# Kernel tuning notes

Measured on AMD Instinct MI355X. Metric: run time of the kernel, lower is better.

## Reference

```python
import jax, jax.numpy as jnp
import numpy as np

NUM_RADIAL = 16
HIDDEN = 128
OUT_DIM = 128
N_LAYERS = 3
N_NODES = 20000
N_EDGES = 640000


def _orthogonal(key, rows, cols):
    # mimic nn.init.orthogonal_ for a [rows, cols] weight
    n = max(rows, cols)
    a = jax.random.normal(key, (n, min(rows, cols)), dtype=jnp.float32)
    q, r = jnp.linalg.qr(a)
    q = q * jnp.sign(jnp.diagonal(r))  # make deterministic-ish sign
    w = q[:rows, :cols] if rows >= cols else q[:cols, :rows].T
    return w.astype(jnp.float32)


def setup_inputs() -> dict:
    key = jax.random.key(0)
    ks = jax.random.split(key, 8)
    distance_representation = jax.random.normal(ks[0], (N_EDGES, NUM_RADIAL), dtype=jnp.float32)
    message = jax.random.normal(ks[1], (N_EDGES, HIDDEN), dtype=jnp.float32)
    edge_index = jax.random.randint(ks[2], (2, N_EDGES), 0, N_NODES, dtype=jnp.int32)
    # parameters (torch Linear stores weight as [out, in])
    Wd = _orthogonal(ks[3], HIDDEN, NUM_RADIAL)          # linear_distance.weight
    layer_keys = jax.random.split(ks[4], N_LAYERS)
    Ws = jnp.stack([_orthogonal(k, HIDDEN, HIDDEN) for k in layer_keys])  # [L, H, H]
    bs = jnp.zeros((N_LAYERS, HIDDEN), dtype=jnp.float32)
    Wout = _orthogonal(ks[5], OUT_DIM, HIDDEN)           # linear_out.weight
    return {
        "distance_representation": distance_representation,
        "message": message,
        "edge_index": edge_index,
        "num_nodes": N_NODES,
        "Wd": Wd,
        "Ws": Ws,
        "bs": bs,
        "Wout": Wout,
    }


def reference(distance_representation, message, edge_index, num_nodes, Wd, Ws, bs, Wout):
    # distance gate: [E, NUM_RADIAL] @ Wd.T -> [E, H]
    gate = distance_representation @ Wd.T
    transformed_message = gate * message                 # [E, H]
    target_index = edge_index[1]
    # edge -> node scatter-add aggregation
    node_embedding = jax.ops.segment_sum(
        transformed_message, target_index, num_segments=num_nodes)  # [N, H]
    for i in range(Ws.shape[0]):
        node_embedding = jax.nn.silu(node_embedding @ Ws[i].T + bs[i])
    return node_embedding @ Wout.T                       # [N, OUT_DIM]
```

## Files before the change

kernel.cpp:

```cpp
#include <hip/hip_runtime.h>

#define HID 128
#define NR  16
#define NLAYER 4
#define CHUNK 16
#define MAXN_LDS 20480
#define NXCD 8

__device__ __forceinline__ float dot4f(float4 a, float4 b) {
    return a.x * b.x + a.y * b.y + a.z * b.z + a.w * b.w;
}

__global__ void hist_kernel(const int* __restrict__ eidx, int* __restrict__ hist, int E) {
    int i = (blockIdx.x * blockDim.x + threadIdx.x) * 4;
    if (i + 4 <= E) {
        int4 v = *(const int4*)(eidx + E + i);
        atomicAdd(&hist[v.x], 1);
        atomicAdd(&hist[v.y], 1);
        atomicAdd(&hist[v.z], 1);
        atomicAdd(&hist[v.w], 1);
    } else {
        for (; i < E; ++i) atomicAdd(&hist[eidx[E + i]], 1);
    }
}

__global__ __launch_bounds__(1024) void prep_kernel(const int* __restrict__ hist,
                                                    int* __restrict__ curs, int N,
                                                    const float* __restrict__ Ws,
                                                    const float* __restrict__ Wout,
                                                    float* __restrict__ WT) {
    const int tid = threadIdx.x;
    if (blockIdx.x > 0) {
        int idx = (blockIdx.x - 1) * 1024 + tid;
        if (idx < NLAYER * HID * HID) {
            int l = idx >> 14;
            int rem = idx & 16383;
            int h = rem >> 7, k = rem & 127;
            const float* src = (l < 3) ? (Ws + ((size_t)l << 14)) : Wout;
            WT[((size_t)l << 14) + (size_t)k * HID + h] = src[(size_t)h * HID + k];
        }
        return;
    }
    __shared__ int sh[MAXN_LDS];
    __shared__ int part[1024];
    const bool use_lds = (N <= MAXN_LDS);
    if (use_lds) {
        for (int i = tid; i < N; i += 1024) sh[i] = hist[i];
        __syncthreads();
    }
    const int per = (N + 1023) >> 10;
    const int base = tid * per;
    int s = 0;
    for (int i = 0; i < per; ++i) {
        int idx = base + i;
        if (idx < N) s += use_lds ? sh[idx] : hist[idx];
    }
    part[tid] = s;
    __syncthreads();
    for (int off = 1; off < 1024; off <<= 1) {
        int v = part[tid];
        int add = (tid >= off) ? part[tid - off] : 0;
        __syncthreads();
        part[tid] = v + add;
        __syncthreads();
    }
    int run = (tid > 0) ? part[tid - 1] : 0;
    for (int i = 0; i < per; ++i) {
        int idx = base + i;
        if (idx < N) {
            curs[idx] = run;
            run += use_lds ? sh[idx] : hist[idx];
        }
    }
}

__global__ void scatter_kernel(const int* __restrict__ eidx, int* __restrict__ curs,
                               int2* __restrict__ pairs, int E) {
    int i = (blockIdx.x * blockDim.x + threadIdx.x) * 4;
    if (i + 4 <= E) {
        int4 v = *(const int4*)(eidx + E + i);
        int p;
        p = atomicAdd(&curs[v.x], 1); pairs[p] = make_int2(i + 0, v.x);
        p = atomicAdd(&curs[v.y], 1); pairs[p] = make_int2(i + 1, v.y);
        p = atomicAdd(&curs[v.z], 1); pairs[p] = make_int2(i + 2, v.z);
        p = atomicAdd(&curs[v.w], 1); pairs[p] = make_int2(i + 3, v.w);
    } else {
        for (; i < E; ++i) {
            int t = eidx[E + i];
            int p = atomicAdd(&curs[t], 1);
            pairs[p] = make_int2(i, t);
        }
    }
}

__global__ __launch_bounds__(256, 4) void gather_kernel(
    const float* __restrict__ dist, const float* __restrict__ msg,
    const float* __restrict__ Wd, const int2* __restrict__ pairs,
    float* __restrict__ node_emb, int E)
{
    __shared__ float sdist[4][CHUNK * NR];

    const int nwg = gridDim.x;
    const int q = nwg / NXCD, r = nwg % NXCD;
    const int xcd = blockIdx.x % NXCD, t = blockIdx.x / NXCD;
    const int bid = (xcd < r) ? (xcd * (q + 1) + t) : (r * (q + 1) + (xcd - r) * q + t);

    const int tid  = threadIdx.x;
    const int lane = tid & 63;
    const int wv   = tid >> 6;
    const long base = ((long)bid * 4 + wv) * CHUNK;
    if (base >= E) return;
    const int cnt = (E - base < CHUNK) ? (int)(E - base) : CHUNK;

    const int base_ch = (lane >> 1) << 2;
    const int kh      = (lane & 1) * 8;
    float4 wdh[4][2];
#pragma unroll
    for (int j = 0; j < 4; ++j) {
        wdh[j][0] = *(const float4*)(Wd + (size_t)(base_ch + j) * NR + kh);
        wdh[j][1] = *(const float4*)(Wd + (size_t)(base_ch + j) * NR + kh + 4);
    }

    int ids[CHUNK], tg[CHUNK];
    if (cnt == CHUNK) {
#pragma unroll
        for (int q2 = 0; q2 < CHUNK / 2; ++q2) {
            int4 v = *(const int4*)(pairs + base + q2 * 2);
            ids[q2*2+0] = v.x; tg[q2*2+0] = v.y;
            ids[q2*2+1] = v.z; tg[q2*2+1] = v.w;
        }
    } else {
#pragma unroll
        for (int i = 0; i < CHUNK; ++i) {
            int2 v = (i < cnt) ? pairs[base + i] : make_int2(0, -1);
            ids[i] = v.x; tg[i] = v.y;
        }
    }

    float dv[CHUNK / 4];
#pragma unroll
    for (int g = 0; g < CHUNK / 4; ++g) {
        int e = ids[g * 4 + (lane >> 4)];
        dv[g] = dist[(size_t)e * NR + (lane & 15)];
    }

    float2 m[CHUNK];
#pragma unroll
    for (int i = 0; i < CHUNK; ++i)
        m[i] = *(const float2*)(msg + (size_t)ids[i] * HID + 2 * lane);

    float* sd = sdist[wv];
#pragma unroll
    for (int g = 0; g < CHUNK / 4; ++g)
        sd[g * 64 + lane] = dv[g];

    const bool odd = (lane & 1);
    float a0 = 0.f, a1 = 0.f;
#pragma unroll
    for (int i = 0; i < CHUNK; ++i) {
        if (i < cnt) {
            const float4* dr = (const float4*)(sd + i * NR + kh);
            float4 d0 = dr[0], d1 = dr[1];
            float p0 = dot4f(d0, wdh[0][0]) + dot4f(d1, wdh[0][1]);
            float p1 = dot4f(d0, wdh[1][0]) + dot4f(d1, wdh[1][1]);
            float p2 = dot4f(d0, wdh[2][0]) + dot4f(d1, wdh[2][1]);
            float p3 = dot4f(d0, wdh[3][0]) + dot4f(d1, wdh[3][1]);
            float s0 = odd ? p0 : p2;
            float s1 = odd ? p1 : p3;
            float r0 = __shfl_xor(s0, 1, 64);
            float r1 = __shfl_xor(s1, 1, 64);
            float g0 = (odd ? p2 : p0) + r0;
            float g1 = (odd ? p3 : p1) + r1;
            a0 += g0 * m[i].x;
            a1 += g1 * m[i].y;
            bool fl = (i == cnt - 1) || (tg[i + 1] != tg[i]);
            if (fl) {
                float* dst = node_emb + (size_t)tg[i] * HID + 2 * lane;
                unsafeAtomicAdd(dst,     a0);
                unsafeAtomicAdd(dst + 1, a1);
                a0 = 0.f; a1 = 0.f;
            }
        }
    }
}

__global__ __launch_bounds__(256) void mlp_kernel(
    float* __restrict__ data, const float* __restrict__ WT,
    const float* __restrict__ bs, int N)
{
    __shared__ float xa[32][132];

    const int tid = threadIdx.x;
    const int nb  = blockIdx.x * 32;
    const int hq  = tid & 31, h0 = hq * 4;
    const int nq  = tid >> 5, n0 = nq * 4;

    for (int i = tid; i < 32 * 32; i += 256) {
        int n = i >> 5, kq = i & 31;
        float4 v = make_float4(0.f, 0.f, 0.f, 0.f);
        if (nb + n < N) v = *(const float4*)(data + (size_t)(nb + n) * HID + kq * 4);
        *(float4*)(&xa[n][kq * 4]) = v;
    }
    __syncthreads();

    for (int l = 0; l < NLAYER; ++l) {
        const float* __restrict__ W = WT + ((size_t)l << 14);
        float acc[4][4];
        if (l < 3) {
            float b[4];
#pragma unroll
            for (int j = 0; j < 4; ++j) b[j] = bs[l * HID + h0 + j];
#pragma unroll
            for (int i = 0; i < 4; ++i)
#pragma unroll
                for (int j = 0; j < 4; ++j) acc[i][j] = b[j];
        } else {
#pragma unroll
            for (int i = 0; i < 4; ++i)
#pragma unroll
                for (int j = 0; j < 4; ++j) acc[i][j] = 0.f;
        }

        for (int k4 = 0; k4 < 32; ++k4) {
            float4 xv[4];
#pragma unroll
            for (int i = 0; i < 4; ++i) xv[i] = *(const float4*)(&xa[n0 + i][k4 * 4]);
            float4 wr[4];
#pragma unroll
            for (int kk = 0; kk < 4; ++kk)
                wr[kk] = *(const float4*)(W + (size_t)(k4 * 4 + kk) * HID + h0);
#pragma unroll
            for (int i = 0; i < 4; ++i) {
                acc[i][0] += xv[i].x * wr[0].x + xv[i].y * wr[1].x + xv[i].z * wr[2].x + xv[i].w * wr[3].x;
                acc[i][1] += xv[i].x * wr[0].y + xv[i].y * wr[1].y + xv[i].z * wr[2].y + xv[i].w * wr[3].y;
                acc[i][2] += xv[i].x * wr[0].z + xv[i].y * wr[1].z + xv[i].z * wr[2].z + xv[i].w * wr[3].z;
                acc[i][3] += xv[i].x * wr[0].w + xv[i].y * wr[1].w + xv[i].z * wr[2].w + xv[i].w * wr[3].w;
            }
        }
        __syncthreads();

        if (l < 3) {
#pragma unroll
            for (int i = 0; i < 4; ++i) {
                float4 y;
                y.x = acc[i][0] / (1.f + __expf(-acc[i][0]));
                y.y = acc[i][1] / (1.f + __expf(-acc[i][1]));
                y.z = acc[i][2] / (1.f + __expf(-acc[i][2]));
                y.w = acc[i][3] / (1.f + __expf(-acc[i][3]));
                *(float4*)(&xa[n0 + i][h0]) = y;
            }
            __syncthreads();
        } else {
#pragma unroll
            for (int i = 0; i < 4; ++i) {
                if (nb + n0 + i < N) {
                    float4 y = make_float4(acc[i][0], acc[i][1], acc[i][2], acc[i][3]);
                    *(float4*)(data + (size_t)(nb + n0 + i) * HID + h0) = y;
                }
            }
        }
    }
}

extern "C" void kernel_launch(void* const* d_in, const int* in_sizes, int n_in,
                              void* d_out, int out_size, void* d_ws, size_t ws_size,
                              hipStream_t stream) {
    const float* dist = (const float*)d_in[0];
    const float* msg  = (const float*)d_in[1];
    const int*   eidx = (const int*)d_in[2];
    const float* Wd   = (const float*)d_in[4];
    const float* Ws   = (const float*)d_in[5];
    const float* bs   = (const float*)d_in[6];
    const float* Wout = (const float*)d_in[7];
    float* out = (float*)d_out;

    const int E = in_sizes[1] / HID;
    const int N = out_size / HID;

    int*   hist   = (int*)d_ws;
    int*   curs   = hist + N;
    size_t pr_off = ((size_t)(2 * N) + 3) & ~(size_t)3;
    int2*  pairs  = (int2*)((int*)d_ws + pr_off);
    size_t wt_off = (pr_off + (size_t)2 * E + 3) & ~(size_t)3;
    float* WT     = (float*)d_ws + wt_off;

    hipMemsetAsync(hist, 0, (size_t)N * sizeof(int), stream);
    hipMemsetAsync(out, 0, (size_t)N * HID * sizeof(float), stream);

    const int qE = (E + 3) / 4;
    const int tblocks = (NLAYER * HID * HID + 1023) / 1024;
    hist_kernel   <<<(qE + 255) / 256, 256, 0, stream>>>(eidx, hist, E);
    prep_kernel   <<<1 + tblocks, 1024, 0, stream>>>(hist, curs, N, Ws, Wout, WT);
    scatter_kernel<<<(qE + 255) / 256, 256, 0, stream>>>(eidx, curs, pairs, E);

    const long waves = ((long)E + CHUNK - 1) / CHUNK;
    gather_kernel <<<(int)((waves + 3) / 4), 256, 0, stream>>>(dist, msg, Wd, pairs, out, E);
    mlp_kernel    <<<(N + 31) / 32, 256, 0, stream>>>(out, WT, bs, N);
}
```

Before: 264.6 us.

## Fuse sort, gather and MLP into one persistent cooperative kernel

Replaces the two memsets and five kernel launches with a single cooperative persistent kernel. Grid-wide syncs separate the zeroing, histogram, multi-block prefix scan, scatter, gather and MLP phases. The aim is to remove launch gaps and the serial single-block scan. The risks are many grid.sync barriers, reduced occupancy (grid capped at 1024 blocks, fixed WPW chunk partitioning) and a scan done by one thread per block.

New measurement: 851.0 us. 222% more time.

```diff
diff --git a/kernel.cpp b/kernel.cpp
--- a/kernel.cpp
+++ b/kernel.cpp
@@ -1,14 +1,304 @@
 #include <hip/hip_runtime.h>
+#include <hip/hip_cooperative_groups.h>
+
+namespace cg = cooperative_groups;
 
 #define HID 128
 #define NR  16
 #define NLAYER 4
 #define CHUNK 16
+#define NXCD 8
 #define MAXN_LDS 20480
-#define NXCD 8
 
 __device__ __forceinline__ float dot4f(float4 a, float4 b) {
     return a.x * b.x + a.y * b.y + a.z * b.z + a.w * b.w;
+}
+
+__global__ __launch_bounds__(256, 4) void fused_kernel(
+    const float* __restrict__ dist, const float* __restrict__ msg,
+    const int* __restrict__ eidx, const float* __restrict__ Wd,
+    const float* __restrict__ Ws, const float* __restrict__ bs,
+    const float* __restrict__ Wout, float* __restrict__ out,
+    int* __restrict__ hist, int* __restrict__ curs, int2* __restrict__ pairs,
+    float* __restrict__ WT, int* __restrict__ bsum,
+    int E, int N, int WPW)
+{
+    cg::grid_group grid = cg::this_grid();
+
+    __shared__ union ShMem {
+        float xa[32][132];
+        int   part[1024];
+        float sdist[4][CHUNK * NR];
+    } sh;
+
+    const int nwg  = gridDim.x;
+    const int tid  = threadIdx.x;
+    const int bid  = blockIdx.x;
+    const int gtid = bid * 256 + tid;
+    const int gstr = nwg * 256;
+
+    for (int i = gtid; i < N; i += gstr) hist[i] = 0;
+    {
+        float4 z = make_float4(0.f, 0.f, 0.f, 0.f);
+        float4* o4 = (float4*)out;
+        const int n4 = N * HID / 4;
+        for (int i = gtid; i < n4; i += gstr) o4[i] = z;
+    }
+    for (int i = gtid; i < NLAYER * HID * HID; i += gstr) {
+        int l = i >> 14;
+        int rem = i & 16383;
+        int h = rem >> 7, k = rem & 127;
+        const float* src = (l < 3) ? (Ws + ((size_t)l << 14)) : Wout;
+        WT[((size_t)l << 14) + (size_t)k * HID + h] = src[(size_t)h * HID + k];
+    }
+    grid.sync();
+
+    for (int i4 = gtid; i4 * 4 < E; i4 += gstr) {
+        int i = i4 * 4;
+        if (i + 4 <= E) {
+            int4 v = *(const int4*)(eidx + E + i);
+            atomicAdd(&hist[v.x], 1);
+            atomicAdd(&hist[v.y], 1);
+            atomicAdd(&hist[v.z], 1);
+            atomicAdd(&hist[v.w], 1);
+        } else {
+            for (; i < E; ++i) atomicAdd(&hist[eidx[E + i]], 1);
+        }
+    }
+    grid.sync();
+
+    const int R = (N + nwg - 1) / nwg;
+    {
+        int idx = bid * R + tid;
+        if (tid < R) sh.part[tid] = (idx < N) ? hist[idx] : 0;
+        __syncthreads();
+        if (tid == 0) {
+            int s = 0;
+            for (int i = 0; i < R; ++i) s += sh.part[i];
+            bsum[bid] = s;
+        }
+    }
+    grid.sync();
+    if (bid == 0) {
+        const int k = (nwg + 255) / 256;
+        int s = 0;
+        for (int i = 0; i < k; ++i) {
+            int idx = tid * k + i;
+            if (idx < nwg) s += bsum[idx];
+        }
+        sh.part[tid] = s;
+        __syncthreads();
+        for (int off = 1; off < 256; off <<= 1) {
+            int x = sh.part[tid];
+            int add = (tid >= off) ? sh.part[tid - off] : 0;
+            __syncthreads();
+            sh.part[tid] = x + add;
+            __syncthreads();
+        }
+        int run = (tid > 0) ? sh.part[tid - 1] : 0;
+        for (int i = 0; i < k; ++i) {
+            int idx = tid * k + i;
+            if (idx < nwg) { int v = bsum[idx]; bsum[idx] = run; run += v; }
+        }
+    }
+    grid.sync();
+    {
+        int idx = bid * R + tid;
+        if (tid < R) sh.part[tid] = (idx < N) ? hist[idx] : 0;
+        __syncthreads();
+        if (tid == 0) {
+            int run = bsum[bid];
+            for (int i = 0; i < R; ++i) {
+                int x = bid * R + i;
+                if (x < N) curs[x] = run;
+                run += sh.part[i];
+            }
+        }
+    }
+    grid.sync();
+
+    for (int i4 = gtid; i4 * 4 < E; i4 += gstr) {
+        int i = i4 * 4;
+        if (i + 4 <= E) {
+            int4 v = *(const int4*)(eidx + E + i);
+            int p;
+            p = atomicAdd(&curs[v.x], 1); pairs[p] = make_int2(i + 0, v.x);
+            p = atomicAdd(&curs[v.y], 1); pairs[p] = make_int2(i + 1, v.y);
+            p = atomicAdd(&curs[v.z], 1); pairs[p] = make_int2(i + 2, v.z);
+            p = atomicAdd(&curs[v.w], 1); pairs[p] = make_int2(i + 3, v.w);
+        } else {
+            for (; i < E; ++i) {
+                int t = eidx[E + i];
+                int p = atomicAdd(&curs[t], 1);
+                pairs[p] = make_int2(i, t);
+            }
+        }
+    }
+    grid.sync();
+
+    {
+        const int cpx = nwg / NXCD;
+        const int bid2 = (bid % NXCD) * cpx + bid / NXCD;
+        const int lane = tid & 63;
+        const int wv   = tid >> 6;
+        const long wi  = (long)bid2 * 4 + wv;
+        const long nchunks = ((long)E + CHUNK - 1) / CHUNK;
+
+        const int base_ch = (lane >> 1) << 2;
+        const int kh      = (lane & 1) * 8;
+        const bool odd    = lane & 1;
+        float4 wdh[4][2];
+#pragma unroll
+        for (int j = 0; j < 4; ++j) {
+            wdh[j][0] = *(const float4*)(Wd + (size_t)(base_ch + j) * NR + kh);
+            wdh[j][1] = *(const float4*)(Wd + (size_t)(base_ch + j) * NR + kh + 4);
+        }
+        float* sd = sh.sdist[wv];
+
+        long c    = wi * WPW;
+        long cend = c + WPW;
+        if (cend > nchunks) cend = nchunks;
+        for (; c < cend; ++c) {
+            const long base = c * CHUNK;
+            const int cnt = ((long)E - base < CHUNK) ? (int)((long)E - base) : CHUNK;
+
+            int ids[CHUNK], tg[CHUNK];
+            if (cnt == CHUNK) {
+#pragma unroll
+                for (int q2 = 0; q2 < CHUNK / 2; ++q2) {
+                    int4 v = *(const int4*)(pairs + base + q2 * 2);
+                    ids[q2*2+0] = v.x; tg[q2*2+0] = v.y;
+                    ids[q2*2+1] = v.z; tg[q2*2+1] = v.w;
+                }
+            } else {
+#pragma unroll
+                for (int i = 0; i < CHUNK; ++i) {
+                    int2 v = (i < cnt) ? pairs[base + i] : make_int2(0, -1);
+                    ids[i] = v.x; tg[i] = v.y;
+                }
+            }
+
+            float dv[CHUNK / 4];
+#pragma unroll
+            for (int g = 0; g < CHUNK / 4; ++g) {
+                int e = ids[g * 4 + (lane >> 4)];
+                dv[g] = dist[(size_t)e * NR + (lane & 15)];
+            }
+
+            float2 m[CHUNK];
+#pragma unroll
+            for (int i = 0; i < CHUNK; ++i)
+                m[i] = *(const float2*)(msg + (size_t)ids[i] * HID + 2 * lane);
+
+#pragma unroll
+            for (int g = 0; g < CHUNK / 4; ++g)
+                sd[g * 64 + lane] = dv[g];
+
+            float a0 = 0.f, a1 = 0.f;
+#pragma unroll
+            for (int i = 0; i < CHUNK; ++i) {
+                if (i < cnt) {
+                    const float4* dr = (const float4*)(sd + i * NR + kh);
+                    float4 d0 = dr[0], d1 = dr[1];
+                    float p0 = dot4f(d0, wdh[0][0]) + dot4f(d1, wdh[0][1]);
+                    float p1 = dot4f(d0, wdh[1][0]) + dot4f(d1, wdh[1][1]);
+                    float p2 = dot4f(d0, wdh[2][0]) + dot4f(d1, wdh[2][1]);
+                    float p3 = dot4f(d0, wdh[3][0]) + dot4f(d1, wdh[3][1]);
+                    float s0 = odd ? p0 : p2;
+                    float s1 = odd ? p1 : p3;
+                    float r0 = __shfl_xor(s0, 1, 64);
+                    float r1 = __shfl_xor(s1, 1, 64);
+                    float g0 = (odd ? p2 : p0) + r0;
+                    float g1 = (odd ? p3 : p1) + r1;
+                    a0 += g0 * m[i].x;
+                    a1 += g1 * m[i].y;
+                    bool fl = (i == cnt - 1) || (tg[i + 1] != tg[i]);
+                    if (fl) {
+                        float* dst = out + (size_t)tg[i] * HID + 2 * lane;
+                        unsafeAtomicAdd(dst,     a0);
+                        unsafeAtomicAdd(dst + 1, a1);
+                        a0 = 0.f; a1 = 0.f;
+                    }
+                }
+            }
+        }
+    }
+    grid.sync();
+
+    {
+        const int ntiles = (N + 31) / 32;
+        const int hq = tid & 31, h0 = hq * 4;
+        const int nq = tid >> 5, n0 = nq * 4;
+        for (int tile = bid; tile < ntiles; tile += nwg) {
+            const int nb = tile * 32;
+            __syncthreads();
+            for (int i = tid; i < 32 * 32; i += 256) {
+                int n = i >> 5, kq = i & 31;
+                float4 v = make_float4(0.f, 0.f, 0.f, 0.f);
+                if (nb + n < N) v = *(const float4*)(out + (size_t)(nb + n) * HID + kq * 4);
+                *(float4*)(&sh.xa[n][kq * 4]) = v;
+            }
+            __syncthreads();
+
+            for (int l = 0; l < NLAYER; ++l) {
+                const float* __restrict__ W = WT + ((size_t)l << 14);
+                float acc[4][4];
+                if (l < 3) {
+                    float b[4];
+#pragma unroll
+                    for (int j = 0; j < 4; ++j) b[j] = bs[l * HID + h0 + j];
+#pragma unroll
+                    for (int i = 0; i < 4; ++i)
+#pragma unroll
+                        for (int j = 0; j < 4; ++j) acc[i][j] = b[j];
+                } else {
+#pragma unroll
+                    for (int i = 0; i < 4; ++i)
+#pragma unroll
+                        for (int j = 0; j < 4; ++j) acc[i][j] = 0.f;
+                }
+
+                for (int k4 = 0; k4 < 32; ++k4) {
+                    float4 xv[4];
+#pragma unroll
+                    for (int i = 0; i < 4; ++i) xv[i] = *(const float4*)(&sh.xa[n0 + i][k4 * 4]);
+                    float4 wr[4];
+#pragma unroll
+                    for (int kk = 0; kk < 4; ++kk)
+                        wr[kk] = *(const float4*)(W + (size_t)(k4 * 4 + kk) * HID + h0);
+#pragma unroll
+                    for (int i = 0; i < 4; ++i) {
+                        acc[i][0] += xv[i].x * wr[0].x + xv[i].y * wr[1].x + xv[i].z * wr[2].x + xv[i].w * wr[3].x;
+                        acc[i][1] += xv[i].x * wr[0].y + xv[i].y * wr[1].y + xv[i].z * wr[2].y + xv[i].w * wr[3].y;
+                        acc[i][2] += xv[i].x * wr[0].z + xv[i].y * wr[1].z + xv[i].z * wr[2].z + xv[i].w * wr[3].z;
+                        acc[i][3] += xv[i].x * wr[0].w + xv[i].y * wr[1].w + xv[i].z * wr[2].w + xv[i].w * wr[3].w;
+                    }
+                }
+                __syncthreads();
+
+                if (l < 3) {
+#pragma unroll
+                    for (int i = 0; i < 4; ++i) {
+                        float4 y;
+                        y.x = acc[i][0] / (1.f + __expf(-acc[i][0]));
+                        y.y = acc[i][1] / (1.f + __expf(-acc[i][1]));
+                        y.z = acc[i][2] / (1.f + __expf(-acc[i][2]));
+                        y.w = acc[i][3] / (1.f + __expf(-acc[i][3]));
+                        *(float4*)(&sh.xa[n0 + i][h0]) = y;
+                    }
+                    __syncthreads();
+                } else {
+#pragma unroll
+                    for (int i = 0; i < 4; ++i) {
+                        if (nb + n0 + i < N) {
+                            float4 y = make_float4(acc[i][0], acc[i][1], acc[i][2], acc[i][3]);
+                            *(float4*)(out + (size_t)(nb + n0 + i) * HID + h0) = y;
+                        }
+                    }
+                }
+            }
+        }
+    }
 }
 
 __global__ void hist_kernel(const int* __restrict__ eidx, int* __restrict__ hist, int E) {
@@ -41,11 +331,11 @@
         }
         return;
     }
-    __shared__ int sh[MAXN_LDS];
+    __shared__ int shh[MAXN_LDS];
     __shared__ int part[1024];
     const bool use_lds = (N <= MAXN_LDS);
     if (use_lds) {
-        for (int i = tid; i < N; i += 1024) sh[i] = hist[i];
+        for (int i = tid; i < N; i += 1024) shh[i] = hist[i];
         __syncthreads();
     }
     const int per = (N + 1023) >> 10;
@@ -53,7 +343,7 @@
     int s = 0;
     for (int i = 0; i < per; ++i) {
         int idx = base + i;
-        if (idx < N) s += use_lds ? sh[idx] : hist[idx];
+        if (idx < N) s += use_lds ? shh[idx] : hist[idx];
     }
     part[tid] = s;
     __syncthreads();
@@ -69,7 +359,7 @@
         int idx = base + i;
         if (idx < N) {
             curs[idx] = run;
-            run += use_lds ? sh[idx] : hist[idx];
+            run += use_lds ? shh[idx] : hist[idx];
         }
     }
 }
@@ -274,8 +564,8 @@
     const float* Wout = (const float*)d_in[7];
     float* out = (float*)d_out;
 
-    const int E = in_sizes[1] / HID;
-    const int N = out_size / HID;
+    int E = in_sizes[1] / HID;
+    int N = out_size / HID;
 
     int*   hist   = (int*)d_ws;
     int*   curs   = hist + N;
@@ -283,17 +573,43 @@
     int2*  pairs  = (int2*)((int*)d_ws + pr_off);
     size_t wt_off = (pr_off + (size_t)2 * E + 3) & ~(size_t)3;
     float* WT     = (float*)d_ws + wt_off;
-
-    hipMemsetAsync(hist, 0, (size_t)N * sizeof(int), stream);
-    hipMemsetAsync(out, 0, (size_t)N * HID * sizeof(float), stream);
-
-    const int qE = (E + 3) / 4;
-    const int tblocks = (NLAYER * HID * HID + 1023) / 1024;
-    hist_kernel   <<<(qE + 255) / 256, 256, 0, stream>>>(eidx, hist, E);
-    prep_kernel   <<<1 + tblocks, 1024, 0, stream>>>(hist, curs, N, Ws, Wout, WT);
-    scatter_kernel<<<(qE + 255) / 256, 256, 0, stream>>>(eidx, curs, pairs, E);
-
-    const long waves = ((long)E + CHUNK - 1) / CHUNK;
-    gather_kernel <<<(int)((waves + 3) / 4), 256, 0, stream>>>(dist, msg, Wd, pairs, out, E);
-    mlp_kernel    <<<(N + 31) / 32, 256, 0, stream>>>(out, WT, bs, N);
-}
+    int*   bsum   = (int*)(WT + NLAYER * HID * HID);
+
+    int maxB = 0;
+    hipError_t qerr = hipOccupancyMaxActiveBlocksPerMultiprocessor(
+        &maxB, reinterpret_cast<const void*>(fused_kernel), 256, 0);
+    int nwg = 0;
+    if (qerr == hipSuccess && maxB > 0) {
+        long g = (long)maxB * 256;
+        if (g > 1024) g = 1024;
+        nwg = (int)(g & ~7L);
+    }
+
+    bool coop_ok = false;
+    if (nwg >= 8) {
+        const long nchunks = ((long)E + CHUNK - 1) / CHUNK;
+        int WPW = (int)((nchunks + (long)nwg * 4 - 1) / ((long)nwg * 4));
+        if (WPW < 1) WPW = 1;
+        void* args[] = { (void*)&dist, (void*)&msg, (void*)&eidx, (void*)&Wd,
+                         (void*)&Ws, (void*)&bs, (void*)&Wout, (void*)&out,
+                         (void*)&hist, (void*)&curs, (void*)&pairs, (void*)&WT,
+                         (void*)&bsum, (void*)&E, (void*)&N, (void*)&WPW };
+        hipError_t lerr = hipLaunchCooperativeKernel(
+            reinterpret_cast<const void*>(fused_kernel), dim3(nwg), dim3(256),
+            args, 0, stream);
+        coop_ok = (lerr == hipSuccess);
+    }
+
+    if (!coop_ok) {
+        hipMemsetAsync(hist, 0, (size_t)N * sizeof(int), stream);
+        hipMemsetAsync(out, 0, (size_t)N * HID * sizeof(float), stream);
+        const int qE = (E + 3) / 4;
+        const int tblocks = (NLAYER * HID * HID + 1023) / 1024;
+        hist_kernel   <<<(qE + 255) / 256, 256, 0, stream>>>(eidx, hist, E);
+        prep_kernel   <<<1 + tblocks, 1024, 0, stream>>>(hist, curs, N, Ws, Wout, WT);
+        scatter_kernel<<<(qE + 255) / 256, 256, 0, stream>>>(eidx, curs, pairs, E);
+        const long waves = ((long)E + CHUNK - 1) / CHUNK;
+        gather_kernel <<<(int)((waves + 3) / 4), 256, 0, stream>>>(dist, msg, Wd, pairs, out, E);
+        mlp_kernel    <<<(N + 31) / 32, 256, 0, stream>>>(out, WT, bs, N);
+    }
+}
```
